# Performance work log

Hardware: AMD Instinct MI355X
Metric: run time of the kernel (lower is better)

## Reference

```python
import jax, jax.numpy as jnp
import numpy as np

B, A, C, M = 16, 76725, 8, 32
EPS = 1e-4


def _iou(b1, b2):
    # b1: [A,4], b2: [M,4]; +1 pixel convention as in the torch source
    lt = jnp.maximum(b1[:, None, :2], b2[None, :, :2])
    rb = jnp.minimum(b1[:, None, 2:], b2[None, :, 2:])
    wh = jnp.clip(rb - lt + 1.0, 0.0)
    inter = wh[..., 0] * wh[..., 1]
    a1 = (b1[:, 2] - b1[:, 0] + 1.0) * (b1[:, 3] - b1[:, 1] + 1.0)
    a2 = (b2[:, 2] - b2[:, 0] + 1.0) * (b2[:, 3] - b2[:, 1] + 1.0)
    return inter / (a1[:, None] + a2[None, :] - inter)


def setup_inputs() -> dict:
    key = jax.random.key(0)
    k1, k2, k3, k4, k5, k6, k7, k8, k9 = jax.random.split(key, 9)
    # anchors: one shared set of boxes, tiled over batch (as RetinaNet does)
    acx = jax.random.uniform(k1, (A,)) * 480.0 + 16.0
    acy = jax.random.uniform(k2, (A,)) * 480.0 + 16.0
    aw = jax.random.uniform(k3, (A,)) * 96.0 + 16.0
    ah = jax.random.uniform(k4, (A,)) * 96.0 + 16.0
    anchor = jnp.stack([acx - 0.5 * aw, acy - 0.5 * ah, acx + 0.5 * aw, acy + 0.5 * ah], -1)
    anchors = jnp.tile(anchor[None], (B, 1, 1))
    # annotations: [B,M,5] = (x1,y1,x2,y2,label); last 8 per image padded with label -1
    x1 = jax.random.uniform(k5, (B, M)) * 380.0
    y1 = jax.random.uniform(k6, (B, M)) * 380.0
    w = jax.random.uniform(k7, (B, M)) * 80.0 + 20.0
    h = jax.random.uniform(k8, (B, M)) * 80.0 + 20.0
    lab = jax.random.randint(k9, (B, M), 0, C).astype(jnp.float32)
    lab = jnp.where(jnp.arange(M)[None, :] < M - 8, lab, -1.0)
    annotations = jnp.stack([x1, y1, x1 + w, y1 + h, lab], -1)
    kc, kr = jax.random.split(jax.random.fold_in(key, 7))
    classifications = jax.random.uniform(kc, (B, A, C), dtype=jnp.float32)
    regressions = jax.random.normal(kr, (B, A, 4), dtype=jnp.float32) * 0.1
    return {
        "classifications": classifications,
        "regressions": regressions,
        "anchors": anchors,
        "annotations": annotations,
    }


def reference(classifications, regressions, anchors, annotations):
    ALPHA, GAMMA = 0.25, 2.0
    dt = classifications.dtype
    nclass = classifications.shape[-1]
    # anchor geometry taken from anchors[0] (as in the torch source)
    anchor0 = anchors[0]
    aw = anchor0[:, 2] - anchor0[:, 0]
    ah = anchor0[:, 3] - anchor0[:, 1]
    acx = anchor0[:, 0] + 0.5 * aw
    acy = anchor0[:, 1] + 0.5 * ah
    norm = jnp.array([0.1, 0.1, 0.2, 0.2], dt)

    def per_image(cls_, reg, anch, ann):
        valid = ann[:, 4] > -0.5  # label != -1
        num_valid = valid.sum()
        iou = _iou(anch, ann[:, :4])  # [A,M]
        iou = jnp.where(valid[None, :], iou, -1.0)  # mask padded annotations
        iou_max = iou.max(axis=1)
        iou_arg = iou.argmax(axis=1)
        p = jnp.clip(cls_, EPS, 1.0 - EPS)  # [A,C]
        assigned = ann[iou_arg]  # [A,5] gather of best annotation per anchor
        pos = iou_max >= 0.4
        npos = pos.sum()
        one_hot = jax.nn.one_hot(assigned[:, 4].astype(jnp.int32), nclass, dtype=dt)
        # targets: -1 ignore, 0 negative (IoU<0.3), one-hot positive (IoU>=0.4)
        targets = jnp.where(pos[:, None], one_hot,
                            jnp.where((iou_max < 0.3)[:, None], 0.0, -1.0))
        is_one = targets == 1.0
        alpha_factor = jnp.where(is_one, ALPHA, 1.0 - ALPHA)
        focal_w = alpha_factor * jnp.where(is_one, 1.0 - p, p) ** GAMMA
        bce = -(targets * jnp.log(p) + (1.0 - targets) * jnp.log1p(-p))
        cls_loss = jnp.where(targets != -1.0, focal_w * bce, 0.0).sum() \
            / jnp.maximum(npos.astype(dt), 1.0)
        w0 = assigned[:, 2] - assigned[:, 0]
        h0 = assigned[:, 3] - assigned[:, 1]
        gcx = assigned[:, 0] + 0.5 * w0
        gcy = assigned[:, 1] + 0.5 * h0
        gw = jnp.clip(w0, 1.0)
        gh = jnp.clip(h0, 1.0)
        t = jnp.stack([(gcx - acx) / aw, (gcy - acy) / ah,
                       jnp.log(gw / aw), jnp.log(gh / ah)], -1) / norm  # [A,4]
        diff = jnp.abs(t - reg)
        sl1 = jnp.where(diff <= 1.0 / 9.0, 0.5 * 9.0 * diff ** 2, diff - 0.5 / 9.0)
        reg_sum = jnp.where(pos[:, None], sl1, 0.0).sum()
        reg_loss = jnp.where(npos > 0,
                             reg_sum / jnp.maximum(npos * 4, 1).astype(dt), 0.0)
        cls_loss = jnp.where(num_valid > 0, cls_loss, 0.0)
        reg_loss = jnp.where(num_valid > 0, reg_loss, 0.0)
        return cls_loss, reg_loss

    cl, rl = jax.vmap(per_image)(classifications, regressions, anchors, annotations)
    return jnp.mean(cl, keepdims=True), jnp.mean(rl, keepdims=True)
```

## Files before the change

### kernel.cpp

```cpp
#include <hip/hip_runtime.h>

#define NB 16
#define NA 76725
#define NC 8
#define NM 32
#define FEPS 1e-4f
#define TPB 256
#define NBX 96
#define APB 800


__global__ __launch_bounds__(TPB, 4) void focal_main(
    const float* __restrict__ cls_,
    const float* __restrict__ reg_,
    const float* __restrict__ anch_,
    const float* __restrict__ ann_,
    float4* __restrict__ partial)
{
    const int b   = blockIdx.y;
    const int xb  = blockIdx.x;
    const int tid = threadIdx.x;

    const float4* __restrict__ anch4 = reinterpret_cast<const float4*>(anch_);
    const float4* __restrict__ reg4  = reinterpret_cast<const float4*>(reg_);
    const float4* __restrict__ cls4  = reinterpret_cast<const float4*>(cls_);

    const int ab = xb * APB;

    const int a0 = ab + tid;
    const bool mk0 = (a0 < NA);
    const size_t b0 = (size_t)b * NA + (mk0 ? a0 : (NA - 1));
    float4 anA = anch4[b0], rgA = reg4[b0], c0A = cls4[b0 * 2], c1A = cls4[b0 * 2 + 1];

    __shared__ float  s_x1[NM], s_y1[NM], s_x21[NM], s_y21[NM], s_a2[NM], s_lab[NM];
    __shared__ float4 s_epi[NM];
    __shared__ int    s_nvp, s_cnt;
    if (tid < 64) {
        bool valid = false;
        float x1 = 0.f, y1 = 0.f, x2 = 0.f, y2 = 0.f, lab = -1.f;
        if (tid < NM) {
            const float* r = ann_ + ((size_t)b * NM + tid) * 5;
            x1 = r[0]; y1 = r[1]; x2 = r[2]; y2 = r[3]; lab = r[4];
            valid = lab > -0.5f;
        }
        const unsigned long long mask = __ballot(valid);
        const int cnt = __popcll(mask);
        if (tid < NM) {
            s_x1[tid] = 3e18f; s_y1[tid] = 3e18f; s_x21[tid] = -3e18f; s_y21[tid] = -3e18f;
            s_a2[tid] = 1.f;   s_lab[tid] = -1.f;
            s_epi[tid] = make_float4(0.f, 0.f, 0.f, 0.f);
        }
        if (valid) {
            const int idx = __popcll(mask & ((1ull << tid) - 1ull));
            s_x1[idx] = x1; s_y1[idx] = y1; s_x21[idx] = x2 + 1.f; s_y21[idx] = y2 + 1.f;
            s_a2[idx] = (x2 - x1 + 1.f) * (y2 - y1 + 1.f);
            s_lab[idx] = lab;
            const float w0 = x2 - x1, h0 = y2 - y1;
            s_epi[idx] = make_float4(x1 + 0.5f * w0, y1 + 0.5f * h0,
                                     __logf(fmaxf(w0, 1.f)), __logf(fmaxf(h0, 1.f)));
        }
        if (tid == 0) { s_nvp = (cnt + 7) & ~7; s_cnt = cnt; }
    }
    __syncthreads();
    int nvp = __builtin_amdgcn_readfirstlane(s_nvp);

    float cls_c = 0.f, reg_c = 0.f;
    unsigned pos_c = 0;

    auto compute = [&](const float4& an, const float4& rg,
                       const float4& cv0, const float4& cv1, bool msk) {
        const float ax = an.x, ay = an.y;
        const float az1 = an.z + 1.f, aw1 = an.w + 1.f;
        const float area1 = (an.z - ax + 1.f) * (an.w - ay + 1.f);

        float ib = 0.f, ub = 1.f;
        int arg = 0;
        #pragma unroll 4
        for (int m = 0; m < nvp; ++m) {
            const float x1 = s_x1[m], y1 = s_y1[m];
            const float x21 = s_x21[m], y21 = s_y21[m];
            const float a2 = s_a2[m];
            const float w = fminf(az1, x21) - fmaxf(ax, x1);
            const float h = fminf(aw1, y21) - fmaxf(ay, y1);
            const float inter = fmaxf(w, 0.f) * fmaxf(h, 0.f);
            const float u = area1 + a2 - inter;
            const bool better = inter * ub > ib * u;
            ib  = better ? inter : ib;
            ub  = better ? u : ub;
            arg = better ? m : arg;
        }
        const bool pos = ib >= 0.4f * ub;
        const bool neg = ib <  0.3f * ub;
        const bool act = (pos || neg) && msk;

        {
            const float pv[8] = {cv0.x, cv0.y, cv0.z, cv0.w, cv1.x, cv1.y, cv1.z, cv1.w};
            float pcl[8];
            float bsum = 0.f;
            #pragma unroll
            for (int c = 0; c < NC; ++c) {
                const float p = fminf(fmaxf(pv[c], FEPS), 1.f - FEPS);
                pcl[c] = p;
                bsum += 0.75f * p * p * (-__logf(1.f - p));
            }
            float contrib = bsum;
            if (pos) {
                const int labi = (int)s_lab[arg];
                const float t0 = (labi & 1) ? pcl[1] : pcl[0];
                const float t1 = (labi & 1) ? pcl[3] : pcl[2];
                const float t2 = (labi & 1) ? pcl[5] : pcl[4];
                const float t3 = (labi & 1) ? pcl[7] : pcl[6];
                const float u0 = (labi & 2) ? t1 : t0;
                const float u1 = (labi & 2) ? t3 : t2;
                const float pt = (labi & 4) ? u1 : u0;
                const float om = 1.f - pt;
                contrib += 0.25f * om * om * (-__logf(pt))
                         - 0.75f * pt * pt * (-__logf(om));
            }
            cls_c += act ? contrib : 0.f;
        }
        if (pos && msk) {
            pos_c += 1;
            const float4 ep = s_epi[arg];
            const float awd = az1 - 1.f - ax;
            const float ahd = aw1 - 1.f - ay;
            const float acx = ax + 0.5f * awd;
            const float acy = ay + 0.5f * ahd;
            const float t0 = __fdividef(ep.x - acx, awd) * 10.f;
            const float t1 = __fdividef(ep.y - acy, ahd) * 10.f;
            const float t2 = (ep.z - __logf(awd)) * 5.f;
            const float t3 = (ep.w - __logf(ahd)) * 5.f;
            const float d0 = fabsf(t0 - rg.x);
            const float d1 = fabsf(t1 - rg.y);
            const float d2 = fabsf(t2 - rg.z);
            const float d3 = fabsf(t3 - rg.w);
            auto sl1 = [](float d) {
                return d <= (1.f / 9.f) ? 4.5f * d * d : d - (0.5f / 9.f);
            };
            reg_c += sl1(d0) + sl1(d1) + sl1(d2) + sl1(d3);
        }
    };

    const int a1 = ab + TPB + tid;
    const bool mk1 = (a1 < NA);
    const size_t b1 = (size_t)b * NA + (mk1 ? a1 : (NA - 1));
    float4 anB = anch4[b1], rgB = reg4[b1], c0B = cls4[b1 * 2], c1B = cls4[b1 * 2 + 1];
    __builtin_amdgcn_sched_barrier(0);
    compute(anA, rgA, c0A, c1A, mk0);

    const int a2i = ab + 2 * TPB + tid;
    const bool mk2 = (a2i < NA);
    const size_t b2 = (size_t)b * NA + (mk2 ? a2i : (NA - 1));
    anA = anch4[b2]; rgA = reg4[b2]; c0A = cls4[b2 * 2]; c1A = cls4[b2 * 2 + 1];
    __builtin_amdgcn_sched_barrier(0);
    compute(anB, rgB, c0B, c1B, mk1);

    bool mk3 = false;
    if (tid < 32) {
        const int a3 = ab + 3 * TPB + tid;
        mk3 = (a3 < NA);
        const size_t b3 = (size_t)b * NA + (mk3 ? a3 : (NA - 1));
        anB = anch4[b3]; rgB = reg4[b3]; c0B = cls4[b3 * 2]; c1B = cls4[b3 * 2 + 1];
    }
    __builtin_amdgcn_sched_barrier(0);
    compute(anA, rgA, c0A, c1A, mk2);
    if (tid < 32) compute(anB, rgB, c0B, c1B, mk3);

    #pragma unroll
    for (int off = 32; off > 0; off >>= 1) {
        cls_c += __shfl_down(cls_c, off);
        reg_c += __shfl_down(reg_c, off);
        pos_c += __shfl_down(pos_c, off);
    }
    __shared__ float    sc[4], sr[4];
    __shared__ unsigned sp[4];
    const int wave = tid >> 6, lane = tid & 63;
    if (lane == 0) { sc[wave] = cls_c; sr[wave] = reg_c; sp[wave] = pos_c; }
    __syncthreads();
    if (tid == 0) {
        const float    c = sc[0] + sc[1] + sc[2] + sc[3];
        const float    r = sr[0] + sr[1] + sr[2] + sr[3];
        const unsigned p = sp[0] + sp[1] + sp[2] + sp[3];
        partial[b * NBX + xb] = make_float4(c, r, (float)p, (float)s_cnt);
    }
}

__global__ __launch_bounds__(64) void focal_finalize(
    const float4* __restrict__ partial, float* __restrict__ out)
{
    const int t = threadIdx.x;
    const int b = t & 15, q = t >> 4;
    float cs = 0.f, rs = 0.f, np = 0.f;
    for (int x = q; x < NBX; x += 4) {
        const float4 v = partial[b * NBX + x];
        cs += v.x; rs += v.y; np += v.z;
    }
    cs += __shfl_down(cs, 32); rs += __shfl_down(rs, 32); np += __shfl_down(np, 32);
    cs += __shfl_down(cs, 16); rs += __shfl_down(rs, 16); np += __shfl_down(np, 16);
    float cl = 0.f, rl = 0.f;
    if (t < 16) {
        const float cnt = partial[b * NBX].w;
        cl = cs / fmaxf(np, 1.f);
        rl = (np > 0.5f) ? rs / (np * 4.f) : 0.f;
        if (cnt < 0.5f) { cl = 0.f; rl = 0.f; }
    }
    #pragma unroll
    for (int off = 8; off > 0; off >>= 1) {
        cl += __shfl_down(cl, off);
        rl += __shfl_down(rl, off);
    }
    if (t == 0) {
        out[0] = cl * (1.f / NB);
        out[1] = rl * (1.f / NB);
    }
}

extern "C" void kernel_launch(void* const* d_in, const int* in_sizes, int n_in,
                              void* d_out, int out_size, void* d_ws, size_t ws_size,
                              hipStream_t stream)
{
    const float* cls_  = (const float*)d_in[0];
    const float* reg_  = (const float*)d_in[1];
    const float* anch_ = (const float*)d_in[2];
    const float* ann_  = (const float*)d_in[3];
    float4* partial = (float4*)d_ws;
    float*  out     = (float*)d_out;

    dim3 grid(NBX, NB);
    focal_main<<<grid, dim3(TPB), 0, stream>>>(cls_, reg_, anch_, ann_, partial);
    focal_finalize<<<1, 64, 0, stream>>>(partial, out);
}
```

Before: 40.60 us.

## Process two anchors per IoU loop iteration and pack annotation boxes as float4

```diff
diff --git a/kernel.cpp b/kernel.cpp
--- a/kernel.cpp
+++ b/kernel.cpp
@@ -6,8 +6,8 @@
 #define NM 32
 #define FEPS 1e-4f
 #define TPB 256
-#define NBX 96
-#define APB 800
+#define APB 1024
+#define NBX ((NA + APB - 1) / APB)
 
 
 __global__ __launch_bounds__(TPB, 4) void focal_main(
@@ -27,12 +27,19 @@
 
     const int ab = xb * APB;
 
-    const int a0 = ab + tid;
-    const bool mk0 = (a0 < NA);
-    const size_t b0 = (size_t)b * NA + (mk0 ? a0 : (NA - 1));
-    float4 anA = anch4[b0], rgA = reg4[b0], c0A = cls4[b0 * 2], c1A = cls4[b0 * 2 + 1];
-
-    __shared__ float  s_x1[NM], s_y1[NM], s_x21[NM], s_y21[NM], s_a2[NM], s_lab[NM];
+    float4 anA[2], rgA[2], c0A[2], c1A[2];
+    bool   mkA[2];
+    #pragma unroll
+    for (int s = 0; s < 2; ++s) {
+        const int a = ab + s * TPB + tid;
+        mkA[s] = (a < NA);
+        const size_t base = (size_t)b * NA + (mkA[s] ? a : (NA - 1));
+        anA[s] = anch4[base]; rgA[s] = reg4[base];
+        c0A[s] = cls4[base * 2]; c1A[s] = cls4[base * 2 + 1];
+    }
+
+    __shared__ float4 s_box[NM];
+    __shared__ float  s_a2[NM], s_lab[NM];
     __shared__ float4 s_epi[NM];
     __shared__ int    s_nvp, s_cnt;
     if (tid < 64) {
@@ -46,13 +53,13 @@
         const unsigned long long mask = __ballot(valid);
         const int cnt = __popcll(mask);
         if (tid < NM) {
-            s_x1[tid] = 3e18f; s_y1[tid] = 3e18f; s_x21[tid] = -3e18f; s_y21[tid] = -3e18f;
+            s_box[tid] = make_float4(3e18f, 3e18f, -3e18f, -3e18f);
             s_a2[tid] = 1.f;   s_lab[tid] = -1.f;
             s_epi[tid] = make_float4(0.f, 0.f, 0.f, 0.f);
         }
         if (valid) {
             const int idx = __popcll(mask & ((1ull << tid) - 1ull));
-            s_x1[idx] = x1; s_y1[idx] = y1; s_x21[idx] = x2 + 1.f; s_y21[idx] = y2 + 1.f;
+            s_box[idx] = make_float4(x1, y1, x2 + 1.f, y2 + 1.f);
             s_a2[idx] = (x2 - x1 + 1.f) * (y2 - y1 + 1.f);
             s_lab[idx] = lab;
             const float w0 = x2 - x1, h0 = y2 - y1;
@@ -67,104 +74,101 @@
     float cls_c = 0.f, reg_c = 0.f;
     unsigned pos_c = 0;
 
-    auto compute = [&](const float4& an, const float4& rg,
-                       const float4& cv0, const float4& cv1, bool msk) {
-        const float ax = an.x, ay = an.y;
-        const float az1 = an.z + 1.f, aw1 = an.w + 1.f;
-        const float area1 = (an.z - ax + 1.f) * (an.w - ay + 1.f);
-
-        float ib = 0.f, ub = 1.f;
-        int arg = 0;
+    auto compute_pair = [&](const float4* an, const float4* rg,
+                            const float4* cv0, const float4* cv1, const bool* mk) {
+        float ax[2], ay[2], az1[2], aw1[2], area1[2], ib[2], ub[2];
+        int   arg[2];
+        #pragma unroll
+        for (int k = 0; k < 2; ++k) {
+            ax[k] = an[k].x; ay[k] = an[k].y;
+            az1[k] = an[k].z + 1.f; aw1[k] = an[k].w + 1.f;
+            area1[k] = (an[k].z - ax[k] + 1.f) * (an[k].w - ay[k] + 1.f);
+            ib[k] = 0.f; ub[k] = 1.f; arg[k] = 0;
+        }
         #pragma unroll 4
         for (int m = 0; m < nvp; ++m) {
-            const float x1 = s_x1[m], y1 = s_y1[m];
-            const float x21 = s_x21[m], y21 = s_y21[m];
+            const float4 q = s_box[m];
             const float a2 = s_a2[m];
-            const float w = fminf(az1, x21) - fmaxf(ax, x1);
-            const float h = fminf(aw1, y21) - fmaxf(ay, y1);
-            const float inter = fmaxf(w, 0.f) * fmaxf(h, 0.f);
-            const float u = area1 + a2 - inter;
-            const bool better = inter * ub > ib * u;
-            ib  = better ? inter : ib;
-            ub  = better ? u : ub;
-            arg = better ? m : arg;
-        }
-        const bool pos = ib >= 0.4f * ub;
-        const bool neg = ib <  0.3f * ub;
-        const bool act = (pos || neg) && msk;
-
-        {
-            const float pv[8] = {cv0.x, cv0.y, cv0.z, cv0.w, cv1.x, cv1.y, cv1.z, cv1.w};
-            float pcl[8];
-            float bsum = 0.f;
             #pragma unroll
-            for (int c = 0; c < NC; ++c) {
-                const float p = fminf(fmaxf(pv[c], FEPS), 1.f - FEPS);
-                pcl[c] = p;
-                bsum += 0.75f * p * p * (-__logf(1.f - p));
+            for (int k = 0; k < 2; ++k) {
+                const float w = fminf(az1[k], q.z) - fmaxf(ax[k], q.x);
+                const float h = fminf(aw1[k], q.w) - fmaxf(ay[k], q.y);
+                const float inter = fmaxf(w, 0.f) * fmaxf(h, 0.f);
+                const float u = area1[k] + a2 - inter;
+                const bool better = inter * ub[k] > ib[k] * u;
+                ib[k]  = better ? inter : ib[k];
+                ub[k]  = better ? u : ub[k];
+                arg[k] = better ? m : arg[k];
             }
-            float contrib = bsum;
-            if (pos) {
-                const int labi = (int)s_lab[arg];
-                const float t0 = (labi & 1) ? pcl[1] : pcl[0];
-                const float t1 = (labi & 1) ? pcl[3] : pcl[2];
-                const float t2 = (labi & 1) ? pcl[5] : pcl[4];
-                const float t3 = (labi & 1) ? pcl[7] : pcl[6];
-                const float u0 = (labi & 2) ? t1 : t0;
-                const float u1 = (labi & 2) ? t3 : t2;
-                const float pt = (labi & 4) ? u1 : u0;
-                const float om = 1.f - pt;
-                contrib += 0.25f * om * om * (-__logf(pt))
-                         - 0.75f * pt * pt * (-__logf(om));
+        }
+        #pragma unroll
+        for (int k = 0; k < 2; ++k) {
+            const bool pos = ib[k] >= 0.4f * ub[k];
+            const bool neg = ib[k] <  0.3f * ub[k];
+            const bool act = (pos || neg) && mk[k];
+            {
+                const float pv[8] = {cv0[k].x, cv0[k].y, cv0[k].z, cv0[k].w,
+                                     cv1[k].x, cv1[k].y, cv1[k].z, cv1[k].w};
+                float pcl[8];
+                float bsum = 0.f;
+                #pragma unroll
+                for (int c = 0; c < NC; ++c) {
+                    const float p = fminf(fmaxf(pv[c], FEPS), 1.f - FEPS);
+                    pcl[c] = p;
+                    bsum += 0.75f * p * p * (-__logf(1.f - p));
+                }
+                float contrib = bsum;
+                if (pos) {
+                    const int labi = (int)s_lab[arg[k]];
+                    const float t0 = (labi & 1) ? pcl[1] : pcl[0];
+                    const float t1 = (labi & 1) ? pcl[3] : pcl[2];
+                    const float t2 = (labi & 1) ? pcl[5] : pcl[4];
+                    const float t3 = (labi & 1) ? pcl[7] : pcl[6];
+                    const float u0 = (labi & 2) ? t1 : t0;
+                    const float u1 = (labi & 2) ? t3 : t2;
+                    const float pt = (labi & 4) ? u1 : u0;
+                    const float om = 1.f - pt;
+                    contrib += 0.25f * om * om * (-__logf(pt))
+                             - 0.75f * pt * pt * (-__logf(om));
+                }
+                cls_c += act ? contrib : 0.f;
             }
-            cls_c += act ? contrib : 0.f;
-        }
-        if (pos && msk) {
-            pos_c += 1;
-            const float4 ep = s_epi[arg];
-            const float awd = az1 - 1.f - ax;
-            const float ahd = aw1 - 1.f - ay;
-            const float acx = ax + 0.5f * awd;
-            const float acy = ay + 0.5f * ahd;
-            const float t0 = __fdividef(ep.x - acx, awd) * 10.f;
-            const float t1 = __fdividef(ep.y - acy, ahd) * 10.f;
-            const float t2 = (ep.z - __logf(awd)) * 5.f;
-            const float t3 = (ep.w - __logf(ahd)) * 5.f;
-            const float d0 = fabsf(t0 - rg.x);
-            const float d1 = fabsf(t1 - rg.y);
-            const float d2 = fabsf(t2 - rg.z);
-            const float d3 = fabsf(t3 - rg.w);
-            auto sl1 = [](float d) {
-                return d <= (1.f / 9.f) ? 4.5f * d * d : d - (0.5f / 9.f);
-            };
-            reg_c += sl1(d0) + sl1(d1) + sl1(d2) + sl1(d3);
+            if (pos && mk[k]) {
+                pos_c += 1;
+                const float4 ep = s_epi[arg[k]];
+                const float awd = az1[k] - 1.f - ax[k];
+                const float ahd = aw1[k] - 1.f - ay[k];
+                const float acx = ax[k] + 0.5f * awd;
+                const float acy = ay[k] + 0.5f * ahd;
+                const float t0 = __fdividef(ep.x - acx, awd) * 10.f;
+                const float t1 = __fdividef(ep.y - acy, ahd) * 10.f;
+                const float t2 = (ep.z - __logf(awd)) * 5.f;
+                const float t3 = (ep.w - __logf(ahd)) * 5.f;
+                const float d0 = fabsf(t0 - rg[k].x);
+                const float d1 = fabsf(t1 - rg[k].y);
+                const float d2 = fabsf(t2 - rg[k].z);
+                const float d3 = fabsf(t3 - rg[k].w);
+                auto sl1 = [](float d) {
+                    return d <= (1.f / 9.f) ? 4.5f * d * d : d - (0.5f / 9.f);
+                };
+                reg_c += sl1(d0) + sl1(d1) + sl1(d2) + sl1(d3);
+            }
         }
     };
 
-    const int a1 = ab + TPB + tid;
-    const bool mk1 = (a1 < NA);
-    const size_t b1 = (size_t)b * NA + (mk1 ? a1 : (NA - 1));
-    float4 anB = anch4[b1], rgB = reg4[b1], c0B = cls4[b1 * 2], c1B = cls4[b1 * 2 + 1];
+    float4 anB[2], rgB[2], c0B[2], c1B[2];
+    bool   mkB[2];
+    #pragma unroll
+    for (int s = 0; s < 2; ++s) {
+        const int a = ab + (2 + s) * TPB + tid;
+        mkB[s] = (a < NA);
+        const size_t base = (size_t)b * NA + (mkB[s] ? a : (NA - 1));
+        anB[s] = anch4[base]; rgB[s] = reg4[base];
+        c0B[s] = cls4[base * 2]; c1B[s] = cls4[base * 2 + 1];
+    }
     __builtin_amdgcn_sched_barrier(0);
-    compute(anA, rgA, c0A, c1A, mk0);
-
-    const int a2i = ab + 2 * TPB + tid;
-    const bool mk2 = (a2i < NA);
-    const size_t b2 = (size_t)b * NA + (mk2 ? a2i : (NA - 1));
-    anA = anch4[b2]; rgA = reg4[b2]; c0A = cls4[b2 * 2]; c1A = cls4[b2 * 2 + 1];
-    __builtin_amdgcn_sched_barrier(0);
-    compute(anB, rgB, c0B, c1B, mk1);
-
-    bool mk3 = false;
-    if (tid < 32) {
-        const int a3 = ab + 3 * TPB + tid;
-        mk3 = (a3 < NA);
-        const size_t b3 = (size_t)b * NA + (mk3 ? a3 : (NA - 1));
-        anB = anch4[b3]; rgB = reg4[b3]; c0B = cls4[b3 * 2]; c1B = cls4[b3 * 2 + 1];
-    }
-    __builtin_amdgcn_sched_barrier(0);
-    compute(anA, rgA, c0A, c1A, mk2);
-    if (tid < 32) compute(anB, rgB, c0B, c1B, mk3);
+    compute_pair(anA, rgA, c0A, c1A, mkA);
+    compute_pair(anB, rgB, c0B, c1B, mkB);
 
     #pragma unroll
     for (int off = 32; off > 0; off >>= 1) {
```

New measurement: 41.04 us. About the same (+1.1%).
